# Kernel optimization log

Measured on AMD Instinct MI355X. Metric: run time of the kernel, lower is better.

The kernel has to match this reference:

```python
import jax, jax.numpy as jnp
import numpy as np

B, IN, HID, N, VAL, ONUM = 2048, 512, 256, 16, 400, 8
CH, CK = 4, 32            # comm heads, comm key/query size
CV = HID                  # comm_value_size forced to hidden_size
K_ACTIVE = 8              # top-k active units


def setup_inputs() -> dict:
    key = jax.random.key(0)
    ks = jax.random.split(key, 12)
    s = 0.02
    return dict(
        x=jax.random.normal(ks[0], (B, 1, IN), jnp.float32),
        hs=jax.random.normal(ks[1], (B, N, HID), jnp.float32),
        option=jax.random.normal(ks[2], (B, 2, ONUM), jnp.float32),
        value_w=jax.random.normal(ks[3], (IN, VAL), jnp.float32) * s,
        value_b=jnp.zeros((VAL,), jnp.float32),
        p_w=jax.random.normal(ks[4], (ONUM, N), jnp.float32),
        p_b=jax.random.normal(ks[5], (N,), jnp.float32),
        x2h_w=jax.random.normal(ks[6], (N, VAL, 3 * HID), jnp.float32) * s,
        h2h_w=jax.random.normal(ks[7], (N, HID, 3 * HID), jnp.float32) * s,
        q_w=jax.random.normal(ks[8], (N, HID, CH * CK), jnp.float32) * s,
        k_w=jax.random.normal(ks[9], (N, HID, CH * CK), jnp.float32) * s,
        v_w=jax.random.normal(ks[10], (N, HID, CH * CV), jnp.float32) * s,
        out_w=jax.random.normal(ks[11], (N, CH * CV, CV), jnp.float32) * s,
    )


def reference(x, hs, option, value_w, value_b, p_w, p_b, x2h_w, h2h_w, q_w, k_w, v_w, out_w):
    b = hs.shape[0]
    # --- input attention (null input appended) ---
    xcat = jnp.concatenate([x, jnp.zeros_like(x)], axis=1)          # (B,2,IN)
    value_layer = xcat @ value_w + value_b                          # (B,2,VAL), 1 input head -> mean is identity
    scores = jnp.einsum('bio,on->bni', option, p_w)                 # (B,N,2)
    p_bias = jnp.stack([jnp.broadcast_to(p_b, (b, N)),
                        jnp.zeros((b, N), x.dtype)], axis=2)        # (B,N,2)
    scores = scores + p_bias
    idx = jax.lax.top_k(scores[:, :, 0], K_ACTIVE)[1]               # (B,k)
    mask = jnp.zeros((b, N), x.dtype).at[jnp.arange(b)[:, None], idx].set(1.0)
    probs = jax.nn.softmax(scores, axis=-1)                         # dropout = identity (eval)
    inputs = jnp.matmul(probs, value_layer) * mask[:, :, None]      # (B,N,VAL)
    # --- grouped GRU ---
    gx = jnp.einsum('bnd,ndh->bnh', inputs, x2h_w)                  # (B,N,3H)
    gh = jnp.einsum('bnd,ndh->bnh', hs, h2h_w)
    i_r, i_i, i_n = jnp.split(gx, 3, axis=2)
    h_r, h_i, h_n = jnp.split(gh, 3, axis=2)
    reset = jax.nn.sigmoid(i_r + h_r)
    inp_g = jax.nn.sigmoid(i_i + h_i)
    newg = jnp.tanh(i_n + reset * h_n)
    hy = newg + inp_g * (hs - newg)                                 # (B,N,HID)
    # --- blocked_grad: identity fwd, grad*mask bwd ---
    m = mask[:, :, None]
    hb = m * hy + jax.lax.stop_gradient((1.0 - m) * hy)
    # --- communication attention ---
    def heads(t, d):  # (B,N,CH*d) -> (B,CH,N,d)
        return t.reshape(b, N, CH, d).transpose(0, 2, 1, 3)
    q = heads(jnp.einsum('bnd,ndh->bnh', hb, q_w), CK)
    k = heads(jnp.einsum('bnd,ndh->bnh', hb, k_w), CK)
    v = heads(jnp.einsum('bnd,ndh->bnh', hb, v_w), CV)
    att = jax.nn.softmax(jnp.einsum('bhnk,bhmk->bhnm', q, k) / (CK ** 0.5), axis=-1)
    att = att * mask[:, None, :, None]                              # mask query rows
    ctx = jnp.einsum('bhnm,bhmd->bhnd', att, v)                     # (B,CH,N,CV)
    ctx = ctx.transpose(0, 2, 1, 3).reshape(b, N, CH * CV)
    ctx = jnp.einsum('bnd,ndh->bnh', ctx, out_w) + hb               # residual
    return m * ctx + (1.0 - m) * hs
```

## Files before the change

### kernel.cpp

```cpp
#include <hip/hip_runtime.h>
#include <hip/hip_bf16.h>
#include <math.h>

#define BATCH 2048
#define INDIM 512
#define HID   256
#define NRIM  16
#define VAL   400
#define ONUM  8
#define CH    4
#define CK    32
#define CV    256
#define KACT  8
#define K2P   704

typedef __hip_bfloat16 hbf;
typedef __attribute__((ext_vector_type(8))) __bf16 bf16x8;
typedef __attribute__((ext_vector_type(4))) float f32x4;

__device__ __forceinline__ float fsig(float x) {
    x = fminf(fmaxf(x, -30.0f), 30.0f);
    return 1.0f / (1.0f + __expf(-x));
}
__device__ __forceinline__ float ftanh_(float x) {
    x = fminf(fmaxf(x, -15.0f), 15.0f);
    float e = __expf(2.0f * x);
    return (e - 1.0f) / (e + 1.0f);
}

__device__ __forceinline__ unsigned packbf(float a, float b) {
    hbf ha = __float2bfloat16(a), hb = __float2bfloat16(b);
    unsigned short ua, ub;
    __builtin_memcpy(&ua, &ha, 2);
    __builtin_memcpy(&ub, &hb, 2);
    return ((unsigned)ub << 16) | ua;
}

#define GLL(g, l) __builtin_amdgcn_global_load_lds(                                   \
    (const __attribute__((address_space(1))) void*)(g),                               \
    (__attribute__((address_space(3))) void*)(l), 16, 0, 0)

__device__ __forceinline__ void t_conv_body(
    const float* __restrict__ src, hbf* __restrict__ dst,
    int K, int C, long s_ns, long d_ns, int dstride,
    int koff, int coff, int cmode, int bx, int by, int bz, float* tileS)
{
    const int c0 = bx * 32, k0 = by * 32;
    const int tx = threadIdx.x & 31, ty = threadIdx.x >> 5;
    float (*tile)[33] = (float(*)[33])tileS;
    const float* s = src + (size_t)bz * s_ns;
    #pragma unroll
    for (int i = 0; i < 4; ++i) {
        int k = k0 + ty + i * 8, c = c0 + tx;
        tile[ty + i * 8][tx] = (k < K && c < C) ? s[(size_t)k * C + c] : 0.0f;
    }
    __syncthreads();
    hbf* d = dst + (size_t)bz * d_ns;
    #pragma unroll
    for (int i = 0; i < 4; ++i) {
        int c = c0 + ty + i * 8, k = k0 + tx;
        if (c < C && k < K) {
            int cc = coff + (cmode ? (c < 512 ? c : c + 256) : c);
            d[(size_t)cc * dstride + koff + k] = __float2bfloat16(tile[tx][ty + i * 8]);
        }
    }
}

__global__ __launch_bounds__(256)
void mega_prep(const float* __restrict__ h2h_w, const float* __restrict__ x2h_w,
               const float* __restrict__ q_w, const float* __restrict__ k_w,
               const float* __restrict__ v_w, const float* __restrict__ out_w,
               const float* __restrict__ value_w, const float* __restrict__ option,
               const float* __restrict__ p_w, const float* __restrict__ p_b,
               const float* __restrict__ x,
               hbf* __restrict__ W2, hbf* __restrict__ Wqkv, hbf* __restrict__ Wout,
               hbf* __restrict__ Wv, float* __restrict__ p0g, float* __restrict__ maskg,
               hbf* __restrict__ xB)
{
    __shared__ float tileS[32 * 33];
    const int id = blockIdx.x;
    const int t  = threadIdx.x;

    if (id < 3072) {
        int l = id, bz = l / 192, rem = l % 192;
        t_conv_body(h2h_w, W2, 256, 768, 196608L, 720896L, K2P, 0, 0, 1,
                    rem % 24, rem / 24, bz, tileS);
    } else if (id < 8064) {
        int l = id - 3072, bz = l / 312, rem = l % 312;
        t_conv_body(x2h_w, W2, 400, 768, 307200L, 720896L, K2P, 256, 0, 0,
                    rem % 24, rem / 24, bz, tileS);
    } else if (id < 8576) {
        int l = id - 8064, bz = l / 32, rem = l % 32;
        t_conv_body(q_w, Wqkv, 256, 128, 32768L, 327680L, 256, 0, 0, 0,
                    rem % 4, rem / 4, bz, tileS);
    } else if (id < 9088) {
        int l = id - 8576, bz = l / 32, rem = l % 32;
        t_conv_body(k_w, Wqkv, 256, 128, 32768L, 327680L, 256, 0, 128, 0,
                    rem % 4, rem / 4, bz, tileS);
    } else if (id < 13184) {
        int l = id - 9088, bz = l / 256, rem = l % 256;
        t_conv_body(v_w, Wqkv, 256, 1024, 262144L, 327680L, 256, 0, 256, 0,
                    rem % 32, rem / 32, bz, tileS);
    } else if (id < 17280) {
        int l = id - 13184, bz = l / 256, rem = l % 256;
        t_conv_body(out_w, Wout, 1024, 256, 262144L, 262144L, 1024, 0, 0, 0,
                    rem % 8, rem / 8, bz, tileS);
    } else if (id < 17488) {
        int l = id - 17280;
        t_conv_body(value_w, Wv, 512, 400, 0L, 0L, 512, 0, 0, 0,
                    l % 13, l / 13, 0, tileS);
    } else if (id < 18672) {
        int l = id - 17488, n = l / 74, idx = (l % 74) * 256 + t;
        uint4 z; z.x = 0; z.y = 0; z.z = 0; z.w = 0;
        uint4* base = (uint4*)(W2 + (size_t)n * 720896);
        if (idx < 14336) {
            int c = 768 + idx / 56, u = 32 + idx % 56;
            base[(size_t)c * 88 + u] = z;
        } else {
            int i2 = idx - 14336;
            int c = i2 / 6, u = 82 + i2 % 6;
            base[(size_t)c * 88 + u] = z;
        }
    } else if (id < 18700) {
        int idx = (id - 18672) * 256 + t;
        int c = 400 + idx / 64, u = idx % 64;
        uint4 z; z.x = 0; z.y = 0; z.z = 0; z.w = 0;
        ((uint4*)Wv)[(size_t)c * 64 + u] = z;
    } else if (id < 19212) {
        int l = id - 18700, n = l / 32, idx = (l % 32) * 256 + t;
        int c = 512 + idx / 32, u = idx % 32;
        uint4 z; z.x = 0; z.y = 0; z.z = 0; z.w = 0;
        ((uint4*)(W2 + (size_t)n * 720896))[(size_t)c * 88 + u] = z;
    } else if (id < 19340) {
        const int bb = t >> 4, n = t & 15;
        const int b  = (id - 19212) * 16 + bb;
        float (*sc)[17] = (float(*)[17])tileS;
        float s0 = p_b[n], s1 = 0.0f;
        #pragma unroll
        for (int o = 0; o < ONUM; ++o) {
            s0 = fmaf(option[(b * 2 + 0) * ONUM + o], p_w[o * NRIM + n], s0);
            s1 = fmaf(option[(b * 2 + 1) * ONUM + o], p_w[o * NRIM + n], s1);
        }
        sc[bb][n] = s0;
        __syncthreads();
        int rank = 0;
        #pragma unroll
        for (int m = 0; m < NRIM; ++m) {
            float sm = sc[bb][m];
            if (sm > s0 || (sm == s0 && m < n)) rank++;
        }
        float mk = (rank < KACT) ? 1.0f : 0.0f;
        float mx = fmaxf(s0, s1);
        float e0 = __expf(s0 - mx), e1 = __expf(s1 - mx);
        p0g[b * NRIM + n]   = e0 / (e0 + e1);
        maskg[b * NRIM + n] = mk;
    } else {
        int i = (id - 19340) * 256 + t;
        float4 v = ((const float4*)x)[i];
        unsigned lo = packbf(v.x, v.y), hi = packbf(v.z, v.w);
        *(uint2*)(xB + (size_t)i * 4) = make_uint2(lo, hi);
    }
}

__global__ __launch_bounds__(256)
void k1b_a2(const float* __restrict__ hs, const float* __restrict__ vl0,
            const float* __restrict__ p0g, const float* __restrict__ maskg,
            const float* __restrict__ value_b, hbf* __restrict__ A2)
{
    const int b = blockIdx.x;
    const int t = threadIdx.x;
    __shared__ float vS[VAL], bS[VAL];
    if (t < 100) {
        ((float4*)vS)[t] = ((const float4*)(vl0 + (size_t)b * 512))[t];
        ((float4*)bS)[t] = ((const float4*)value_b)[t];
    }
    __syncthreads();

    for (int n = 0; n < NRIM; ++n) {
        size_t ro = ((size_t)b * NRIM + n) * K2P;
        float p0 = p0g[b * NRIM + n], mk = maskg[b * NRIM + n];
        if (t < 128) {
            float2 hv = ((const float2*)(hs + ((size_t)b * NRIM + n) * HID))[t];
            ((unsigned*)(A2 + ro))[t] = packbf(hv.x, hv.y);
        } else if (t < 152) {
            ((unsigned*)(A2 + ro + 656))[t - 128] = 0;
        }
        if (t < 200) {
            float a0 = mk * (p0 * vS[2 * t]     + (1.0f - p0) * bS[2 * t]);
            float a1 = mk * (p0 * vS[2 * t + 1] + (1.0f - p0) * bS[2 * t + 1]);
            ((unsigned*)(A2 + ro + 256))[t] = packbf(a0, a1);
        }
    }
}

__device__ __forceinline__ void gemm_core64(const hbf* __restrict__ A, long lda,
                                            const hbf* __restrict__ B, long ldb,
                                            int K, short* As, short* Bs, f32x4 acc[4][4])
{
    const int t = threadIdx.x;
    const int w = t >> 6, lane = t & 63;
    const int l15 = lane & 15, l4 = lane >> 4;
    const int rl = lane >> 3;
    const int gu = (lane & 7) ^ rl;
    const int l7 = l15 & 7;

    const hbf* pa[4];
    const hbf* pb[4];
    #pragma unroll
    for (int q = 0; q < 4; ++q) {
        int row = q * 32 + w * 8 + rl;
        pa[q] = A + (size_t)row * lda + gu * 8;
        pb[q] = B + (size_t)row * ldb + gu * 8;
    }

    for (int kk = 0; kk < K; kk += 64) {
        __syncthreads();
        #pragma unroll
        for (int q = 0; q < 4; ++q) {
            GLL(pa[q], As + (q * 32 + w * 8) * 64);
            GLL(pb[q], Bs + (q * 32 + w * 8) * 64);
            pa[q] += 64; pb[q] += 64;
        }
        __syncthreads();

        const int wr = w >> 1, wc = w & 1;
        #pragma unroll
        for (int ks = 0; ks < 2; ++ks) {
            const int p = (ks * 4 + l4) ^ l7;
            bf16x8 af[4], bfr[4];
            #pragma unroll
            for (int m = 0; m < 4; ++m)
                af[m] = *(const bf16x8*)(As + (wr * 64 + m * 16 + l15) * 64 + p * 8);
            #pragma unroll
            for (int nb = 0; nb < 4; ++nb)
                bfr[nb] = *(const bf16x8*)(Bs + (wc * 64 + nb * 16 + l15) * 64 + p * 8);
            #pragma unroll
            for (int m = 0; m < 4; ++m)
                #pragma unroll
                for (int nb = 0; nb < 4; ++nb)
                    acc[m][nb] = __builtin_amdgcn_mfma_f32_16x16x32_bf16(af[m], bfr[nb], acc[m][nb], 0, 0, 0);
        }
    }
}

__global__ __launch_bounds__(256)
void k1v(const hbf* __restrict__ xB, const hbf* __restrict__ Wv,
         const float* __restrict__ value_b, float* __restrict__ vl0)
{
    __shared__ __align__(16) short As[128 * 64];
    __shared__ __align__(16) short Bs[128 * 64];
    const int m0 = (blockIdx.x >> 2) * 128;
    const int c0 = (blockIdx.x & 3) * 128;

    const hbf* A = xB + (size_t)m0 * INDIM;
    const hbf* B = Wv + (size_t)c0 * INDIM;

    f32x4 acc[4][4];
    f32x4 zz = {0.0f, 0.0f, 0.0f, 0.0f};
    #pragma unroll
    for (int m = 0; m < 4; ++m)
        #pragma unroll
        for (int nb = 0; nb < 4; ++nb) acc[m][nb] = zz;

    gemm_core64(A, INDIM, B, INDIM, INDIM, As, Bs, acc);

    const int t = threadIdx.x;
    const int w = t >> 6, lane = t & 63, l15 = lane & 15, l4 = lane >> 4;
    const int wr = w >> 1, wc = w & 1;
    #pragma unroll
    for (int nb = 0; nb < 4; ++nb) {
        int col = c0 + wc * 64 + nb * 16 + l15;
        float bias = (col < VAL) ? value_b[col] : 0.0f;
        #pragma unroll
        for (int m = 0; m < 4; ++m)
            #pragma unroll
            for (int j = 0; j < 4; ++j) {
                int row = m0 + wr * 64 + m * 16 + l4 * 4 + j;
                vl0[(size_t)row * 512 + col] = acc[m][nb][j] + bias;
            }
    }
}

__global__ __launch_bounds__(256)
void k2g(const hbf* __restrict__ A2, const hbf* __restrict__ W2, hbf* __restrict__ hyB)
{
    __shared__ __align__(16) short As[128 * 64];
    __shared__ __align__(16) short Bs[128 * 64];
    const int id = blockIdx.x;
    const int xcd = id & 7, idx = id >> 3;
    const int n  = xcd + ((idx >> 7) << 3);
    const int rem = idx & 127;
    const int m0 = (rem >> 3) * 128;
    const int c0 = rem & 7;

    const hbf* A = A2 + (size_t)n * K2P + (size_t)m0 * (NRIM * K2P);
    const hbf* Bb = W2 + (size_t)n * (1024 * K2P);

    const int t = threadIdx.x;
    const int w = t >> 6, lane = t & 63;
    const int l15 = lane & 15, l4 = lane >> 4;
    const int rl = lane >> 3;
    const int gu = (lane & 7) ^ rl;
    const int l7 = l15 & 7;
    const int wr = w >> 1, wc = w & 1;

    f32x4 acc[4][4];
    f32x4 zz = {0.0f, 0.0f, 0.0f, 0.0f};
    #pragma unroll
    for (int m = 0; m < 4; ++m)
        #pragma unroll
        for (int nb = 0; nb < 4; ++nb) acc[m][nb] = zz;

    const hbf* pa[4];
    const hbf* pb[4];
    int gq[4];
    #pragma unroll
    for (int q = 0; q < 4; ++q) {
        int row = q * 32 + w * 8 + rl;
        int wrow = ((row >> 4) & 3) * 256 + c0 * 32 + ((row >> 6) << 4) + (row & 15);
        pa[q] = A + (size_t)row * (NRIM * K2P) + gu * 8;
        pb[q] = Bb + (size_t)wrow * K2P + gu * 8;
        gq[q] = (2 * q + (w >> 1)) & 3;
    }

    for (int kk = 0; kk < 256; kk += 64) {
        __syncthreads();
        #pragma unroll
        for (int q = 0; q < 4; ++q) {
            GLL(pa[q], As + (q * 32 + w * 8) * 64);
            if (gq[q] != 2) GLL(pb[q], Bs + (q * 32 + w * 8) * 64);
            pa[q] += 64; pb[q] += 64;
        }
        __syncthreads();
        #pragma unroll
        for (int ks = 0; ks < 2; ++ks) {
            const int p = (ks * 4 + l4) ^ l7;
            bf16x8 af[4];
            #pragma unroll
            for (int m = 0; m < 4; ++m)
                af[m] = *(const bf16x8*)(As + (wr * 64 + m * 16 + l15) * 64 + p * 8);
            bf16x8 b0 = *(const bf16x8*)(Bs + (wc * 64 + 0 * 16 + l15) * 64 + p * 8);
            bf16x8 b1 = *(const bf16x8*)(Bs + (wc * 64 + 1 * 16 + l15) * 64 + p * 8);
            bf16x8 b3 = *(const bf16x8*)(Bs + (wc * 64 + 3 * 16 + l15) * 64 + p * 8);
            #pragma unroll
            for (int m = 0; m < 4; ++m) {
                acc[m][0] = __builtin_amdgcn_mfma_f32_16x16x32_bf16(af[m], b0, acc[m][0], 0, 0, 0);
                acc[m][1] = __builtin_amdgcn_mfma_f32_16x16x32_bf16(af[m], b1, acc[m][1], 0, 0, 0);
                acc[m][3] = __builtin_amdgcn_mfma_f32_16x16x32_bf16(af[m], b3, acc[m][3], 0, 0, 0);
            }
        }
    }

    for (int kk = 256; kk < K2P; kk += 64) {
        __syncthreads();
        #pragma unroll
        for (int q = 0; q < 4; ++q) {
            GLL(pa[q], As + (q * 32 + w * 8) * 64);
            if (gq[q] != 3) GLL(pb[q], Bs + (q * 32 + w * 8) * 64);
            pa[q] += 64; pb[q] += 64;
        }
        __syncthreads();
        #pragma unroll
        for (int ks = 0; ks < 2; ++ks) {
            const int p = (ks * 4 + l4) ^ l7;
            bf16x8 af[4];
            #pragma unroll
            for (int m = 0; m < 4; ++m)
                af[m] = *(const bf16x8*)(As + (wr * 64 + m * 16 + l15) * 64 + p * 8);
            bf16x8 b0 = *(const bf16x8*)(Bs + (wc * 64 + 0 * 16 + l15) * 64 + p * 8);
            bf16x8 b1 = *(const bf16x8*)(Bs + (wc * 64 + 1 * 16 + l15) * 64 + p * 8);
            bf16x8 b2 = *(const bf16x8*)(Bs + (wc * 64 + 2 * 16 + l15) * 64 + p * 8);
            #pragma unroll
            for (int m = 0; m < 4; ++m) {
                acc[m][0] = __builtin_amdgcn_mfma_f32_16x16x32_bf16(af[m], b0, acc[m][0], 0, 0, 0);
                acc[m][1] = __builtin_amdgcn_mfma_f32_16x16x32_bf16(af[m], b1, acc[m][1], 0, 0, 0);
                acc[m][2] = __builtin_amdgcn_mfma_f32_16x16x32_bf16(af[m], b2, acc[m][2], 0, 0, 0);
            }
        }
    }

    const int col = c0 * 32 + wc * 16 + l15;
    #pragma unroll
    for (int m = 0; m < 4; ++m)
        #pragma unroll
        for (int j = 0; j < 4; ++j) {
            int row = m0 + wr * 64 + m * 16 + l4 * 4 + j;
            size_t ridx = (size_t)row * NRIM + n;
            float reset = fsig(acc[m][0][j]);
            float inp   = fsig(acc[m][1][j]);
            float newg  = ftanh_(acc[m][2][j] + reset * acc[m][3][j]);
            float h     = __bfloat162float(A2[ridx * K2P + col]);
            hyB[ridx * HID + col] = __float2bfloat16(newg + inp * (h - newg));
        }
}

__global__ __launch_bounds__(256)
void k3g(const hbf* __restrict__ hyB, const hbf* __restrict__ Wqkv, hbf* __restrict__ qkv)
{
    __shared__ __align__(16) short As[128 * 64];
    __shared__ __align__(16) short Bs[128 * 64];
    const int id = blockIdx.x;
    const int xcd = id & 7, idx = id >> 3;
    const int n  = xcd + (idx / 160) * 8;
    const int rem = idx % 160;
    const int m0 = (rem / 10) * 128;
    const int c0 = (rem % 10) * 128;

    const hbf* A = hyB + (size_t)n * HID + (size_t)m0 * (NRIM * HID);
    const hbf* B = Wqkv + (size_t)n * (1280 * 256) + (size_t)c0 * 256;

    f32x4 acc[4][4];
    f32x4 zz = {0.0f, 0.0f, 0.0f, 0.0f};
    #pragma unroll
    for (int m = 0; m < 4; ++m)
        #pragma unroll
        for (int nb = 0; nb < 4; ++nb) acc[m][nb] = zz;

    gemm_core64(A, NRIM * HID, B, 256, 256, As, Bs, acc);

    const int t = threadIdx.x;
    const int w = t >> 6, lane = t & 63, l15 = lane & 15, l4 = lane >> 4;
    const int wr = w >> 1, wc = w & 1;
    #pragma unroll
    for (int m = 0; m < 4; ++m)
        #pragma unroll
        for (int nb = 0; nb < 4; ++nb) {
            int col = c0 + wc * 64 + nb * 16 + l15;
            int rb  = m0 + wr * 64 + m * 16 + l4 * 4;
            #pragma unroll
            for (int j = 0; j < 4; ++j)
                qkv[((size_t)(rb + j) * 16 + n) * 1280 + col] = __float2bfloat16(acc[m][nb][j]);
        }
}

__global__ __launch_bounds__(256)
void k4_attn(const hbf* __restrict__ qkv, const float* __restrict__ maskg,
             hbf* __restrict__ ctx)
{
    const int b = blockIdx.x;
    const int t = threadIdx.x;
    const int w = t >> 6, lane = t & 63;
    const int l15 = lane & 15, g = lane >> 4;

    __shared__ hbf vS[16 * 1024];

    {
        const int r = t >> 4, c = t & 15;
        const uint4* src = (const uint4*)(qkv + (size_t)(b * 16 + r) * 1280 + 256);
        uint4* dst = (uint4*)(vS + r * 1024);
        #pragma unroll
        for (int i = 0; i < 8; ++i) dst[c + i * 16] = src[c + i * 16];
    }

    const hbf* qrow = qkv + (size_t)(b * 16 + l15) * 1280 + w * 32 + g * 8;
    bf16x8 qf = *(const bf16x8*)(qrow);
    bf16x8 kf = *(const bf16x8*)(qrow + 128);
    f32x4 s = {0.f, 0.f, 0.f, 0.f};
    s = __builtin_amdgcn_mfma_f32_16x16x32_bf16(kf, qf, s, 0, 0, 0);

    const float scale = 0.17677669529663687f;
    float v0 = s[0] * scale, v1 = s[1] * scale, v2 = s[2] * scale, v3 = s[3] * scale;
    float mx = fmaxf(fmaxf(v0, v1), fmaxf(v2, v3));
    mx = fmaxf(mx, __shfl_xor(mx, 16));
    mx = fmaxf(mx, __shfl_xor(mx, 32));
    float e0 = __expf(v0 - mx), e1 = __expf(v1 - mx);
    float e2 = __expf(v2 - mx), e3 = __expf(v3 - mx);
    float sm = e0 + e1 + e2 + e3;
    sm += __shfl_xor(sm, 16);
    sm += __shfl_xor(sm, 32);
    float inv = maskg[b * NRIM + l15] / sm;

    unsigned u0 = packbf(e0 * inv, e1 * inv);
    unsigned u1 = packbf(e2 * inv, e3 * inv);
    int sl = l15 + (g << 5);
    unsigned f0 = __shfl((int)u0, sl);
    unsigned f1 = __shfl((int)u1, sl);
    unsigned f2 = __shfl((int)u0, sl + 16);
    unsigned f3 = __shfl((int)u1, sl + 16);
    if (lane >= 32) { f0 = 0; f1 = 0; f2 = 0; f3 = 0; }
    union { unsigned u[4]; bf16x8 v; } pf;
    pf.u[0] = f0; pf.u[1] = f1; pf.u[2] = f2; pf.u[3] = f3;

    __syncthreads();

    const unsigned short* vsu = (const unsigned short*)vS;
    const int vbase = (8 * (g & 1)) * 1024 + w * 256 + l15;
    hbf* crow = ctx + (size_t)(b * 16 + l15) * 1024 + w * 256 + g * 4;
    #pragma unroll
    for (int dc = 0; dc < 16; ++dc) {
        union { unsigned short u[8]; bf16x8 v; } vf;
        #pragma unroll
        for (int e = 0; e < 8; ++e)
            vf.u[e] = vsu[vbase + e * 1024 + dc * 16];
        f32x4 o = {0.f, 0.f, 0.f, 0.f};
        o = __builtin_amdgcn_mfma_f32_16x16x32_bf16(vf.v, pf.v, o, 0, 0, 0);
        unsigned lo = packbf(o[0], o[1]);
        unsigned hi = packbf(o[2], o[3]);
        *(uint2*)(crow + dc * 16) = make_uint2(lo, hi);
    }
}

__global__ __launch_bounds__(256)
void k5g(const hbf* __restrict__ ctx, const hbf* __restrict__ Wout,
         const hbf* __restrict__ hyB, const float* __restrict__ hs,
         const float* __restrict__ maskg, float* __restrict__ out)
{
    __shared__ __align__(16) short As[128 * 64];
    __shared__ __align__(16) short Bs[128 * 64];
    const int id = blockIdx.x;
    const int xcd = id & 7, idx = id >> 3;
    const int n  = xcd + ((idx >> 5) << 3);
    const int rem = idx & 31;
    const int m0 = (rem >> 1) * 128;
    const int c0 = (rem & 1) * 128;

    const hbf* A = ctx + (size_t)n * 1024 + (size_t)m0 * (NRIM * 1024);
    const hbf* B = Wout + (size_t)n * (256 * 1024) + (size_t)c0 * 1024;

    f32x4 acc[4][4];
    f32x4 zz = {0.0f, 0.0f, 0.0f, 0.0f};
    #pragma unroll
    for (int m = 0; m < 4; ++m)
        #pragma unroll
        for (int nb = 0; nb < 4; ++nb) acc[m][nb] = zz;

    gemm_core64(A, NRIM * 1024, B, 1024, 1024, As, Bs, acc);

    const int t = threadIdx.x;
    const int w = t >> 6, lane = t & 63, l15 = lane & 15, l4 = lane >> 4;
    const int wr = w >> 1, wc = w & 1;
    #pragma unroll
    for (int m = 0; m < 4; ++m)
        #pragma unroll
        for (int nb = 0; nb < 4; ++nb) {
            int col = c0 + wc * 64 + nb * 16 + l15;
            #pragma unroll
            for (int j = 0; j < 4; ++j) {
                int row = m0 + wr * 64 + m * 16 + l4 * 4 + j;
                size_t idx2 = ((size_t)row * NRIM + n) * HID + col;
                float mk = maskg[row * NRIM + n];
                out[idx2] = (mk > 0.5f) ? (acc[m][nb][j] + __bfloat162float(hyB[idx2]))
                                        : hs[idx2];
            }
        }
}

extern "C" void kernel_launch(void* const* d_in, const int* in_sizes, int n_in,
                              void* d_out, int out_size, void* d_ws, size_t ws_size,
                              hipStream_t stream) {
    const float* x       = (const float*)d_in[0];
    const float* hs      = (const float*)d_in[1];
    const float* option  = (const float*)d_in[2];
    const float* value_w = (const float*)d_in[3];
    const float* value_b = (const float*)d_in[4];
    const float* p_w     = (const float*)d_in[5];
    const float* p_b     = (const float*)d_in[6];
    const float* x2h_w   = (const float*)d_in[7];
    const float* h2h_w   = (const float*)d_in[8];
    const float* q_w     = (const float*)d_in[9];
    const float* k_w     = (const float*)d_in[10];
    const float* v_w     = (const float*)d_in[11];
    const float* out_w   = (const float*)d_in[12];
    float* out = (float*)d_out;

    char* ws = (char*)d_ws;
    hbf* A2   = (hbf*)(ws);
    hbf* ctx  = (hbf*)(ws);
    size_t off = 67108864;
    hbf* qkv  = (hbf*)(ws + off);
    off += 83886080;
    hbf* W2   = (hbf*)(ws + off); off += 23068672;
    hbf* Wqkv = (hbf*)(ws + off); off += 10485760;
    hbf* Wout = (hbf*)(ws + off); off += 8388608;
    hbf* hyB  = (hbf*)(ws + off); off += 16777216;
    float* vl0   = (float*)(ws + off); off += 4194304;
    hbf* xB   = (hbf*)(ws + off); off += 2097152;
    hbf* Wv   = (hbf*)(ws + off); off += 524288;
    float* p0g   = (float*)(ws + off); off += 131072;
    float* maskg = (float*)(ws + off); off += 131072;

    mega_prep<<<dim3(20364), dim3(256), 0, stream>>>(
        h2h_w, x2h_w, q_w, k_w, v_w, out_w, value_w, option, p_w, p_b, x,
        W2, Wqkv, Wout, Wv, p0g, maskg, xB);

    k1v<<<dim3(64), dim3(256), 0, stream>>>(xB, Wv, value_b, vl0);
    k1b_a2<<<dim3(BATCH), dim3(256), 0, stream>>>(hs, vl0, p0g, maskg, value_b, A2);

    k2g<<<dim3(2048), dim3(256), 0, stream>>>(A2, W2, hyB);

    k3g<<<dim3(2560), dim3(256), 0, stream>>>(hyB, Wqkv, qkv);

    k4_attn<<<dim3(BATCH), dim3(256), 0, stream>>>(qkv, maskg, ctx);

    k5g<<<dim3(512), dim3(256), 0, stream>>>(ctx, Wout, hyB, hs, maskg, out);
}
```

Baseline: 229.9 us.

## Compact active rows per unit and skip inactive rows in output projection GEMM

k1b_a2 now builds a per-unit list of active batch rows with atomics. k5g runs its out_w GEMM as a gathered GEMM over only those rows, using smaller 64-row tiles and early exit for empty tiles. The passthrough copy of hs for inactive units moves into k4_attn. Only about half the rows are active, so roughly half the GEMM work is skipped, at the cost of gathered loads, atomics and an extra memset.

```diff
diff --git a/kernel.cpp b/kernel.cpp
--- a/kernel.cpp
+++ b/kernel.cpp
@@ -165,7 +165,8 @@
 __global__ __launch_bounds__(256)
 void k1b_a2(const float* __restrict__ hs, const float* __restrict__ vl0,
             const float* __restrict__ p0g, const float* __restrict__ maskg,
-            const float* __restrict__ value_b, hbf* __restrict__ A2)
+            const float* __restrict__ value_b, hbf* __restrict__ A2,
+            int* __restrict__ rowcnt, int* __restrict__ rowlist)
 {
     const int b = blockIdx.x;
     const int t = threadIdx.x;
@@ -173,6 +174,13 @@
     if (t < 100) {
         ((float4*)vS)[t] = ((const float4*)(vl0 + (size_t)b * 512))[t];
         ((float4*)bS)[t] = ((const float4*)value_b)[t];
+    }
+    if (t >= 128 && t < 144) {
+        int n = t - 128;
+        if (maskg[b * NRIM + n] > 0.5f) {
+            int pos = atomicAdd(&rowcnt[n], 1);
+            rowlist[n * 2048 + pos] = b;
+        }
     }
     __syncthreads();
 
@@ -435,7 +443,8 @@
 
 __global__ __launch_bounds__(256)
 void k4_attn(const hbf* __restrict__ qkv, const float* __restrict__ maskg,
-             hbf* __restrict__ ctx)
+             const float* __restrict__ hs, hbf* __restrict__ ctx,
+             float* __restrict__ out)
 {
     const int b = blockIdx.x;
     const int t = threadIdx.x;
@@ -450,6 +459,14 @@
         uint4* dst = (uint4*)(vS + r * 1024);
         #pragma unroll
         for (int i = 0; i < 8; ++i) dst[c + i * 16] = src[c + i * 16];
+    }
+
+    #pragma unroll
+    for (int n2 = 0; n2 < NRIM; ++n2) {
+        if (maskg[b * NRIM + n2] < 0.5f) {
+            size_t r = ((size_t)b * NRIM + n2) * HID + t;
+            out[r] = hs[r];
+        }
     }
 
     const hbf* qrow = qkv + (size_t)(b * 16 + l15) * 1280 + w * 32 + g * 8;
@@ -502,45 +519,98 @@
 
 __global__ __launch_bounds__(256)
 void k5g(const hbf* __restrict__ ctx, const hbf* __restrict__ Wout,
-         const hbf* __restrict__ hyB, const float* __restrict__ hs,
-         const float* __restrict__ maskg, float* __restrict__ out)
-{
-    __shared__ __align__(16) short As[128 * 64];
+         const hbf* __restrict__ hyB, const int* __restrict__ rowlist,
+         const int* __restrict__ rowcnt, float* __restrict__ out)
+{
+    __shared__ __align__(16) short As[64 * 64];
     __shared__ __align__(16) short Bs[128 * 64];
     const int id = blockIdx.x;
     const int xcd = id & 7, idx = id >> 3;
-    const int n  = xcd + ((idx >> 5) << 3);
-    const int rem = idx & 31;
-    const int m0 = (rem >> 1) * 128;
+    const int n  = xcd + ((idx >> 6) << 3);
+    const int rem = idx & 63;
+    const int m0 = (rem >> 1) * 64;
     const int c0 = (rem & 1) * 128;
 
-    const hbf* A = ctx + (size_t)n * 1024 + (size_t)m0 * (NRIM * 1024);
-    const hbf* B = Wout + (size_t)n * (256 * 1024) + (size_t)c0 * 1024;
-
-    f32x4 acc[4][4];
+    const int cnt = rowcnt[n];
+    if (m0 >= cnt) return;
+
+    const int t = threadIdx.x;
+    const int w = t >> 6, lane = t & 63;
+    const int l15 = lane & 15, l4 = lane >> 4;
+    const int rl = lane >> 3;
+    const int gu = (lane & 7) ^ rl;
+    const int l7 = l15 & 7;
+    const int wr = w >> 1, wc = w & 1;
+
+    const hbf* Bb = Wout + (size_t)n * (256 * 1024) + (size_t)c0 * 1024;
+    const int* rl_n = rowlist + n * 2048;
+
+    const hbf* pa[2];
+    #pragma unroll
+    for (int q = 0; q < 2; ++q) {
+        int i = m0 + q * 32 + w * 8 + rl;
+        if (i > cnt - 1) i = cnt - 1;
+        int b = rl_n[i];
+        pa[q] = ctx + ((size_t)b * 16 + n) * 1024 + gu * 8;
+    }
+    const hbf* pb[4];
+    #pragma unroll
+    for (int q = 0; q < 4; ++q) {
+        int row = q * 32 + w * 8 + rl;
+        pb[q] = Bb + (size_t)row * 1024 + gu * 8;
+    }
+
+    f32x4 acc[2][4];
     f32x4 zz = {0.0f, 0.0f, 0.0f, 0.0f};
     #pragma unroll
-    for (int m = 0; m < 4; ++m)
+    for (int m = 0; m < 2; ++m)
         #pragma unroll
         for (int nb = 0; nb < 4; ++nb) acc[m][nb] = zz;
 
-    gemm_core64(A, NRIM * 1024, B, 1024, 1024, As, Bs, acc);
-
-    const int t = threadIdx.x;
-    const int w = t >> 6, lane = t & 63, l15 = lane & 15, l4 = lane >> 4;
-    const int wr = w >> 1, wc = w & 1;
-    #pragma unroll
-    for (int m = 0; m < 4; ++m)
-        #pragma unroll
-        for (int nb = 0; nb < 4; ++nb) {
-            int col = c0 + wc * 64 + nb * 16 + l15;
-            #pragma unroll
-            for (int j = 0; j < 4; ++j) {
-                int row = m0 + wr * 64 + m * 16 + l4 * 4 + j;
-                size_t idx2 = ((size_t)row * NRIM + n) * HID + col;
-                float mk = maskg[row * NRIM + n];
-                out[idx2] = (mk > 0.5f) ? (acc[m][nb][j] + __bfloat162float(hyB[idx2]))
-                                        : hs[idx2];
+    for (int kk = 0; kk < 1024; kk += 64) {
+        __syncthreads();
+        #pragma unroll
+        for (int q = 0; q < 2; ++q) {
+            GLL(pa[q], As + (q * 32 + w * 8) * 64);
+            pa[q] += 64;
+        }
+        #pragma unroll
+        for (int q = 0; q < 4; ++q) {
+            GLL(pb[q], Bs + (q * 32 + w * 8) * 64);
+            pb[q] += 64;
+        }
+        __syncthreads();
+        #pragma unroll
+        for (int ks = 0; ks < 2; ++ks) {
+            const int p = (ks * 4 + l4) ^ l7;
+            bf16x8 af[2], bfr[4];
+            #pragma unroll
+            for (int m = 0; m < 2; ++m)
+                af[m] = *(const bf16x8*)(As + (wr * 32 + m * 16 + l15) * 64 + p * 8);
+            #pragma unroll
+            for (int nb = 0; nb < 4; ++nb)
+                bfr[nb] = *(const bf16x8*)(Bs + (wc * 64 + nb * 16 + l15) * 64 + p * 8);
+            #pragma unroll
+            for (int m = 0; m < 2; ++m)
+                #pragma unroll
+                for (int nb = 0; nb < 4; ++nb)
+                    acc[m][nb] = __builtin_amdgcn_mfma_f32_16x16x32_bf16(af[m], bfr[nb], acc[m][nb], 0, 0, 0);
+        }
+    }
+
+    #pragma unroll
+    for (int m = 0; m < 2; ++m)
+        #pragma unroll
+        for (int j = 0; j < 4; ++j) {
+            int i = m0 + wr * 32 + m * 16 + l4 * 4 + j;
+            if (i < cnt) {
+                int b = rl_n[i];
+                #pragma unroll
+                for (int nb = 0; nb < 4; ++nb) {
+                    int col = c0 + wc * 64 + nb * 16 + l15;
+                    size_t idx2 = ((size_t)b * 16 + n) * 256 + col;
+                    out[idx2] = acc[m][nb][j] + __bfloat162float(hyB[idx2]);
+                }
             }
         }
 }
@@ -578,19 +648,24 @@
     hbf* Wv   = (hbf*)(ws + off); off += 524288;
     float* p0g   = (float*)(ws + off); off += 131072;
     float* maskg = (float*)(ws + off); off += 131072;
+    int* rowcnt  = (int*)(ws + off);   off += 256;
+    int* rowlist = (int*)(ws + off);   off += 131072;
+
+    hipMemsetAsync(rowcnt, 0, 64, stream);
 
     mega_prep<<<dim3(20364), dim3(256), 0, stream>>>(
         h2h_w, x2h_w, q_w, k_w, v_w, out_w, value_w, option, p_w, p_b, x,
         W2, Wqkv, Wout, Wv, p0g, maskg, xB);
 
     k1v<<<dim3(64), dim3(256), 0, stream>>>(xB, Wv, value_b, vl0);
-    k1b_a2<<<dim3(BATCH), dim3(256), 0, stream>>>(hs, vl0, p0g, maskg, value_b, A2);
+    k1b_a2<<<dim3(BATCH), dim3(256), 0, stream>>>(hs, vl0, p0g, maskg, value_b, A2,
+                                                  rowcnt, rowlist);
 
     k2g<<<dim3(2048), dim3(256), 0, stream>>>(A2, W2, hyB);
 
     k3g<<<dim3(2560), dim3(256), 0, stream>>>(hyB, Wqkv, qkv);
 
-    k4_attn<<<dim3(BATCH), dim3(256), 0, stream>>>(qkv, maskg, ctx);
-
-    k5g<<<dim3(512), dim3(256), 0, stream>>>(ctx, Wout, hyB, hs, maskg, out);
-}
+    k4_attn<<<dim3(BATCH), dim3(256), 0, stream>>>(qkv, maskg, hs, ctx, out);
+
+    k5g<<<dim3(1024), dim3(256), 0, stream>>>(ctx, Wout, hyB, rowlist, rowcnt, out);
+}
```

New measurement: 250.2 us. 8.8% more time.
